# Performance work log

Measured on AMD Instinct MI355X. Metric: run time of the kernel, lower is better.

## Reference

```python
import jax, jax.numpy as jnp
import numpy as np

LAMBDA = 0.01

def setup_inputs() -> dict:
    key = jax.random.key(0)
    x = jax.random.normal(key, (32, 16384, 64), dtype=jnp.float32)
    return {"x": x}

def reference(x):
    # x: (B, N, D)
    B, N, D = x.shape
    mean = jnp.mean(x, axis=1, keepdims=True)          # (B, 1, D)
    diffs = x - mean                                    # (B, N, D)
    # Fused covariance: sum of centered outer products == GEMM, no (B,N,D,D) blowup
    cov = jnp.einsum('bnd,bne->bde', diffs, diffs) / (N - 1)  # (B, D, D)
    cov = cov + LAMBDA * jnp.eye(D, dtype=x.dtype)
    # torch.unique on the flattened symmetric matrices == globally sorted set of the
    # B * D*(D+1)/2 distinct entries (duplicates only arise from symmetry, prob-1 for
    # continuous inputs). Extract upper triangle per batch, then global sort.
    iu, ju = jnp.triu_indices(D)
    tri = cov[:, iu, ju]                                # (B, d_out)
    d_out = D * (D + 1) // 2
    return jnp.sort(tri.reshape(-1)).reshape(B, d_out)
```

## Files before the change

### kernel.cpp

```cpp
#include <hip/hip_runtime.h>
#include <stdint.h>


#define BATCHES 32
#define NSAMP   16384
#define DIM     64
#define LAMBDA  0.01f
#define NTRI    2080
#define NOUT    (BATCHES * NTRI)

#define CHUNKS_PER_BATCH 32
#define SAMP_PER_BLOCK   (NSAMP / CHUNKS_PER_BATCH)
#define SAMP_PER_WAVE    (SAMP_PER_BLOCK / 4)
#define LDS_ROW_BYTES    72
#define LDS_WAVE_BYTES   (DIM * LDS_ROW_BYTES)

typedef __attribute__((ext_vector_type(4))) float f32x4;
typedef __attribute__((ext_vector_type(8))) short s16x8;

__device__ __forceinline__ uint32_t f32_to_bf16(float f) {
    uint32_t u = __builtin_bit_cast(uint32_t, f);
    return (u + 0x7FFFu + ((u >> 16) & 1u)) >> 16;
}

__device__ __forceinline__ uint32_t sort_key(float v) {
    uint32_t u = __builtin_bit_cast(uint32_t, v);
    return u ^ (uint32_t)(((int32_t)u >> 31) | 0x80000000u);
}

__global__ __launch_bounds__(256, 4) void cov_kernel(const float* __restrict__ x,
                                                     float* __restrict__ S,
                                                     float* __restrict__ Msum) {
    __shared__ union {
        char  trans[4][LDS_WAVE_BYTES];
        float red[2][64][41];
    } lds_u;

    const int tid  = threadIdx.x;
    const int wave = tid >> 6;
    const int lane = tid & 63;
    const int b     = blockIdx.x / CHUNKS_PER_BATCH;
    const int chunk = blockIdx.x % CHUNKS_PER_BATCH;
    const int n_start = chunk * SAMP_PER_BLOCK + wave * SAMP_PER_WAVE;
    const float* xb = x + ((size_t)b * NSAMP + n_start) * DIM;

    char* lds = lds_u.trans[wave];

    const int l15  = lane & 15;
    const int quad = lane >> 4;
    char* frag_base = lds + l15 * LDS_ROW_BYTES + quad * 16;
    char* wrow = lds + lane * LDS_ROW_BYTES;

    f32x4 acc[10];
#pragma unroll
    for (int t = 0; t < 10; ++t) acc[t] = (f32x4){0.f, 0.f, 0.f, 0.f};
    float sum = 0.f;

    for (int kc = 0; kc < SAMP_PER_WAVE / 32; ++kc) {
#pragma unroll
        for (int h = 0; h < 2; ++h) {
            const float* xs = xb + (kc * 32 + h * 16) * DIM + lane;
            float v[16];
#pragma unroll
            for (int j = 0; j < 16; ++j) v[j] = xs[j * DIM];
#pragma unroll
            for (int j = 0; j < 16; ++j) sum += v[j];
            uint32_t p[8];
#pragma unroll
            for (int j = 0; j < 8; ++j)
                p[j] = f32_to_bf16(v[2 * j]) | (f32_to_bf16(v[2 * j + 1]) << 16);
#pragma unroll
            for (int j = 0; j < 4; ++j)
                *(uint2*)(wrow + h * 32 + j * 8) = make_uint2(p[2 * j], p[2 * j + 1]);
        }

        s16x8 frag[4];
#pragma unroll
        for (int t = 0; t < 4; ++t) {
            uint2 lo = *(uint2*)(frag_base + t * 16 * LDS_ROW_BYTES);
            uint2 hi = *(uint2*)(frag_base + t * 16 * LDS_ROW_BYTES + 8);
            uint4 u = make_uint4(lo.x, lo.y, hi.x, hi.y);
            frag[t] = __builtin_bit_cast(s16x8, u);
        }

        acc[0] = __builtin_amdgcn_mfma_f32_16x16x32_bf16(frag[0], frag[0], acc[0], 0, 0, 0);
        acc[1] = __builtin_amdgcn_mfma_f32_16x16x32_bf16(frag[0], frag[1], acc[1], 0, 0, 0);
        acc[2] = __builtin_amdgcn_mfma_f32_16x16x32_bf16(frag[0], frag[2], acc[2], 0, 0, 0);
        acc[3] = __builtin_amdgcn_mfma_f32_16x16x32_bf16(frag[0], frag[3], acc[3], 0, 0, 0);
        acc[4] = __builtin_amdgcn_mfma_f32_16x16x32_bf16(frag[1], frag[1], acc[4], 0, 0, 0);
        acc[5] = __builtin_amdgcn_mfma_f32_16x16x32_bf16(frag[1], frag[2], acc[5], 0, 0, 0);
        acc[6] = __builtin_amdgcn_mfma_f32_16x16x32_bf16(frag[1], frag[3], acc[6], 0, 0, 0);
        acc[7] = __builtin_amdgcn_mfma_f32_16x16x32_bf16(frag[2], frag[2], acc[7], 0, 0, 0);
        acc[8] = __builtin_amdgcn_mfma_f32_16x16x32_bf16(frag[2], frag[3], acc[8], 0, 0, 0);
        acc[9] = __builtin_amdgcn_mfma_f32_16x16x32_bf16(frag[3], frag[3], acc[9], 0, 0, 0);
    }

    __syncthreads();
    if (wave == 1 || wave == 3) {
        int slot = wave >> 1;
#pragma unroll
        for (int t = 0; t < 10; ++t)
#pragma unroll
            for (int r = 0; r < 4; ++r) lds_u.red[slot][lane][t * 4 + r] = acc[t][r];
    }
    __syncthreads();
    if (wave == 0 || wave == 2) {
        int slot = wave >> 1;
#pragma unroll
        for (int t = 0; t < 10; ++t)
#pragma unroll
            for (int r = 0; r < 4; ++r) acc[t][r] += lds_u.red[slot][lane][t * 4 + r];
    }
    __syncthreads();
    if (wave == 2) {
#pragma unroll
        for (int t = 0; t < 10; ++t)
#pragma unroll
            for (int r = 0; r < 4; ++r) lds_u.red[0][lane][t * 4 + r] = acc[t][r];
    }
    __syncthreads();

    atomicAdd(&Msum[b * DIM + lane], sum);

    if (wave == 0) {
#pragma unroll
        for (int t = 0; t < 10; ++t)
#pragma unroll
            for (int r = 0; r < 4; ++r) acc[t][r] += lds_u.red[0][lane][t * 4 + r];

        const int tmi[10] = {0, 0, 0, 0, 1, 1, 1, 2, 2, 3};
        const int tni[10] = {0, 1, 2, 3, 1, 2, 3, 2, 3, 3};
        float* Sb = S + b * DIM * DIM;
#pragma unroll
        for (int t = 0; t < 10; ++t) {
            int d0 = tmi[t] * 16 + quad * 4;
            int e  = tni[t] * 16 + l15;
#pragma unroll
            for (int r = 0; r < 4; ++r)
                atomicAdd(&Sb[(d0 + r) * DIM + e], acc[t][r]);
        }
    }
}

__global__ void finalize_kernel(const float* __restrict__ S,
                                const float* __restrict__ Msum,
                                float* __restrict__ tri,
                                uint32_t* __restrict__ hist) {
    int t = blockIdx.x * blockDim.x + threadIdx.x;
    int b = t >> 12, de = t & 4095, d = de >> 6, e = de & 63;
    if (d > e) return;
    float ssum = S[b * 4096 + d * 64 + e];
    float md = Msum[b * 64 + d], me = Msum[b * 64 + e];
    float v = (ssum - md * me * (1.0f / NSAMP)) * (1.0f / (NSAMP - 1));
    if (d == e) v += LAMBDA;
    int p = d * 64 - (d * (d + 1)) / 2 + e;
    tri[b * NTRI + p] = v;
    atomicAdd(&hist[sort_key(v) >> 16], 1u);
}

__global__ __launch_bounds__(256) void scanA_kernel(const uint32_t* __restrict__ hist,
                                                    uint32_t* __restrict__ blocksums) {
    __shared__ uint32_t s[256];
    int tid = threadIdx.x;
    s[tid] = hist[blockIdx.x * 256 + tid];
    __syncthreads();
    for (int off = 128; off > 0; off >>= 1) {
        if (tid < off) s[tid] += s[tid + off];
        __syncthreads();
    }
    if (tid == 0) blocksums[blockIdx.x] = s[0];
}

__global__ __launch_bounds__(256) void scanB_kernel(const uint32_t* __restrict__ hist,
                                                    const uint32_t* __restrict__ blocksums,
                                                    uint32_t* __restrict__ offsets,
                                                    uint2* __restrict__ wl_small,
                                                    uint2* __restrict__ wl_large,
                                                    uint32_t* __restrict__ counts) {
    __shared__ uint32_t bs[256];
    __shared__ uint32_t sc[256];
    int tid = threadIdx.x, bid = blockIdx.x;

    bs[tid] = blocksums[tid];
    __syncthreads();
    for (int off = 1; off < 256; off <<= 1) {
        uint32_t a = (tid >= off) ? bs[tid - off] : 0u;
        __syncthreads();
        bs[tid] += a;
        __syncthreads();
    }
    uint32_t base = (bid > 0) ? bs[bid - 1] : 0u;

    uint32_t v = hist[bid * 256 + tid];
    sc[tid] = v;
    __syncthreads();
    for (int off = 1; off < 256; off <<= 1) {
        uint32_t a = (tid >= off) ? sc[tid - off] : 0u;
        __syncthreads();
        sc[tid] += a;
        __syncthreads();
    }
    uint32_t excl = base + sc[tid] - v;
    offsets[bid * 256 + tid] = excl;
    if (v >= 2u) {
        if (v <= 64u) {
            uint32_t w = atomicAdd(&counts[0], 1u);
            wl_small[w] = make_uint2(excl, v);
        } else {
            uint32_t w = atomicAdd(&counts[1], 1u);
            wl_large[w] = make_uint2(excl, v);
        }
    }
}

__global__ void scatter_kernel(const float* __restrict__ tri,
                               uint32_t* __restrict__ offsets,
                               float* __restrict__ out) {
    int i = blockIdx.x * blockDim.x + threadIdx.x;
    if (i >= NOUT) return;
    float v = tri[i];
    uint32_t pos = atomicAdd(&offsets[sort_key(v) >> 16], 1u);
    out[pos] = v;
}

__global__ __launch_bounds__(256) void runsort_small_kernel(float* __restrict__ out,
                                                            const uint2* __restrict__ wl,
                                                            const uint32_t* __restrict__ counts) {
    uint32_t nw = counts[0];
    int wave = threadIdx.x >> 6, lane = threadIdx.x & 63;
    for (uint32_t r = blockIdx.x * 4 + wave; r < nw; r += gridDim.x * 4) {
        uint2 e = wl[r];
        uint32_t start = e.x, cnt = e.y;
        float v = (lane < (int)cnt) ? out[start + lane] : __builtin_inff();
#pragma unroll
        for (uint32_t k = 2; k <= 64; k <<= 1)
            for (uint32_t j = k >> 1; j > 0; j >>= 1) {
                float p = __shfl_xor(v, (int)j, 64);
                bool keepmin = (((lane & k) == 0u) == ((lane & j) == 0u));
                v = keepmin ? fminf(v, p) : fmaxf(v, p);
            }
        if (lane < (int)cnt) out[start + lane] = v;
    }
}

#define SORT_CAP 8192
__global__ __launch_bounds__(256) void runsort_large_kernel(float* __restrict__ out,
                                                            const uint2* __restrict__ wl,
                                                            const uint32_t* __restrict__ counts) {
    __shared__ float buf[SORT_CAP];
    uint32_t nw = counts[1];
    for (uint32_t w = blockIdx.x; w < nw; w += gridDim.x) {
        uint2 ent = wl[w];
        uint32_t start = ent.x, cnt = ent.y;
        if (cnt > SORT_CAP) continue;
        uint32_t m = 1;
        while (m < cnt) m <<= 1;
        for (uint32_t i = threadIdx.x; i < m; i += blockDim.x)
            buf[i] = (i < cnt) ? out[start + i] : __builtin_inff();
        __syncthreads();
        for (uint32_t k = 2; k <= m; k <<= 1) {
            for (uint32_t j = k >> 1; j > 0; j >>= 1) {
                for (uint32_t i = threadIdx.x; i < m; i += blockDim.x) {
                    uint32_t ixj = i ^ j;
                    if (ixj > i) {
                        float a = buf[i], c = buf[ixj];
                        bool up = ((i & k) == 0u);
                        if ((a > c) == up) { buf[i] = c; buf[ixj] = a; }
                    }
                }
                __syncthreads();
            }
        }
        for (uint32_t i = threadIdx.x; i < cnt; i += blockDim.x)
            out[start + i] = buf[i];
        __syncthreads();
    }
}

extern "C" void kernel_launch(void* const* d_in, const int* in_sizes, int n_in,
                              void* d_out, int out_size, void* d_ws, size_t ws_size,
                              hipStream_t stream) {
    const float* x = (const float*)d_in[0];
    float* out = (float*)d_out;
    char* ws = (char*)d_ws;

    float*    S         = (float*)(ws);
    float*    Msum      = (float*)(ws + 524288);
    uint32_t* hist      = (uint32_t*)(ws + 532480);
    uint32_t* counts    = (uint32_t*)(ws + 794624);
    uint32_t* offsets   = (uint32_t*)(ws + 794688);
    uint32_t* blocksums = (uint32_t*)(ws + 1056832);
    float*    tri       = (float*)(ws + 1057856);
    uint2*    wl_small  = (uint2*)(ws + 1324096);
    uint2*    wl_large  = (uint2*)(ws + 1590336);

    hipMemsetAsync(d_ws, 0, 794688, stream);
    cov_kernel<<<BATCHES * CHUNKS_PER_BATCH, 256, 0, stream>>>(x, S, Msum);
    finalize_kernel<<<(BATCHES * 4096) / 256, 256, 0, stream>>>(S, Msum, tri, hist);
    scanA_kernel<<<256, 256, 0, stream>>>(hist, blocksums);
    scanB_kernel<<<256, 256, 0, stream>>>(hist, blocksums, offsets, wl_small, wl_large, counts);
    scatter_kernel<<<260, 256, 0, stream>>>(tri, offsets, out);
    runsort_small_kernel<<<128, 256, 0, stream>>>(out, wl_small, counts);
    runsort_large_kernel<<<64, 256, 0, stream>>>(out, wl_large, counts);
}
```

Baseline: 366.2 us.

## Replace global atomic covariance accumulation with per-block partials and fused reduce

Each covariance block now writes its raw MFMA accumulator tile and its column sums to a private partials buffer, with no float atomics into S and Msum. A new per-batch reduce kernel sums the 32 chunk partials, applies the mean correction, scaling and lambda, and fills the triangle and histogram. This removes atomic contention, the separate finalize pass, and a larger memset. It costs an extra ~10 MB partials write and read, and the reduce runs on only 32 blocks. The old atomic path is kept as a fallback when the workspace is too small.

```diff
diff --git a/kernel.cpp b/kernel.cpp
--- a/kernel.cpp
+++ b/kernel.cpp
@@ -14,6 +14,7 @@
 #define SAMP_PER_WAVE    (SAMP_PER_BLOCK / 4)
 #define LDS_ROW_BYTES    72
 #define LDS_WAVE_BYTES   (DIM * LDS_ROW_BYTES)
+#define PARTIAL_STRIDE   2624
 
 typedef __attribute__((ext_vector_type(4))) float f32x4;
 typedef __attribute__((ext_vector_type(8))) short s16x8;
@@ -28,14 +29,20 @@
     return u ^ (uint32_t)(((int32_t)u >> 31) | 0x80000000u);
 }
 
-__global__ __launch_bounds__(256, 4) void cov_kernel(const float* __restrict__ x,
-                                                     float* __restrict__ S,
-                                                     float* __restrict__ Msum) {
-    __shared__ union {
+__constant__ const int c_tmi[10] = {0, 0, 0, 0, 1, 1, 1, 2, 2, 3};
+__constant__ const int c_tni[10] = {0, 1, 2, 3, 1, 2, 3, 2, 3, 3};
+
+struct CovLds {
+    union {
         char  trans[4][LDS_WAVE_BYTES];
         float red[2][64][41];
-    } lds_u;
-
+    } u;
+    float msum_red[4][64];
+};
+
+template <typename EpilogueFn>
+__device__ __forceinline__ void cov_body(const float* __restrict__ x, CovLds& L,
+                                         EpilogueFn epi) {
     const int tid  = threadIdx.x;
     const int wave = tid >> 6;
     const int lane = tid & 63;
@@ -44,7 +51,7 @@
     const int n_start = chunk * SAMP_PER_BLOCK + wave * SAMP_PER_WAVE;
     const float* xb = x + ((size_t)b * NSAMP + n_start) * DIM;
 
-    char* lds = lds_u.trans[wave];
+    char* lds = L.u.trans[wave];
 
     const int l15  = lane & 15;
     const int quad = lane >> 4;
@@ -95,13 +102,14 @@
         acc[9] = __builtin_amdgcn_mfma_f32_16x16x32_bf16(frag[3], frag[3], acc[9], 0, 0, 0);
     }
 
+    L.msum_red[wave][lane] = sum;
     __syncthreads();
     if (wave == 1 || wave == 3) {
         int slot = wave >> 1;
 #pragma unroll
         for (int t = 0; t < 10; ++t)
 #pragma unroll
-            for (int r = 0; r < 4; ++r) lds_u.red[slot][lane][t * 4 + r] = acc[t][r];
+            for (int r = 0; r < 4; ++r) L.u.red[slot][lane][t * 4 + r] = acc[t][r];
     }
     __syncthreads();
     if (wave == 0 || wave == 2) {
@@ -109,35 +117,90 @@
 #pragma unroll
         for (int t = 0; t < 10; ++t)
 #pragma unroll
-            for (int r = 0; r < 4; ++r) acc[t][r] += lds_u.red[slot][lane][t * 4 + r];
+            for (int r = 0; r < 4; ++r) acc[t][r] += L.u.red[slot][lane][t * 4 + r];
     }
     __syncthreads();
     if (wave == 2) {
 #pragma unroll
         for (int t = 0; t < 10; ++t)
 #pragma unroll
-            for (int r = 0; r < 4; ++r) lds_u.red[0][lane][t * 4 + r] = acc[t][r];
-    }
-    __syncthreads();
-
-    atomicAdd(&Msum[b * DIM + lane], sum);
-
+            for (int r = 0; r < 4; ++r) L.u.red[0][lane][t * 4 + r] = acc[t][r];
+    }
+    __syncthreads();
     if (wave == 0) {
 #pragma unroll
         for (int t = 0; t < 10; ++t)
 #pragma unroll
-            for (int r = 0; r < 4; ++r) acc[t][r] += lds_u.red[0][lane][t * 4 + r];
-
-        const int tmi[10] = {0, 0, 0, 0, 1, 1, 1, 2, 2, 3};
-        const int tni[10] = {0, 1, 2, 3, 1, 2, 3, 2, 3, 3};
+            for (int r = 0; r < 4; ++r) acc[t][r] += L.u.red[0][lane][t * 4 + r];
+        float msum_tot = L.msum_red[0][lane] + L.msum_red[1][lane] +
+                         L.msum_red[2][lane] + L.msum_red[3][lane];
+        epi(b, lane, quad, l15, acc, msum_tot);
+    }
+}
+
+__global__ __launch_bounds__(256, 4) void cov_kernel_p(const float* __restrict__ x,
+                                                       float* __restrict__ partials) {
+    __shared__ CovLds L;
+    float* Pb = partials + (size_t)blockIdx.x * PARTIAL_STRIDE;
+    cov_body(x, L, [&](int b, int lane, int quad, int l15, f32x4* acc, float msum) {
+#pragma unroll
+        for (int t = 0; t < 10; ++t)
+#pragma unroll
+            for (int r = 0; r < 4; ++r)
+                Pb[t * 256 + r * 64 + lane] = acc[t][r];
+        Pb[2560 + lane] = msum;
+    });
+}
+
+__global__ __launch_bounds__(256, 4) void cov_kernel_a(const float* __restrict__ x,
+                                                       float* __restrict__ S,
+                                                       float* __restrict__ Msum) {
+    __shared__ CovLds L;
+    cov_body(x, L, [&](int b, int lane, int quad, int l15, f32x4* acc, float msum) {
         float* Sb = S + b * DIM * DIM;
 #pragma unroll
         for (int t = 0; t < 10; ++t) {
-            int d0 = tmi[t] * 16 + quad * 4;
-            int e  = tni[t] * 16 + l15;
+            int d0 = c_tmi[t] * 16 + quad * 4;
+            int e  = c_tni[t] * 16 + l15;
 #pragma unroll
             for (int r = 0; r < 4; ++r)
                 atomicAdd(&Sb[(d0 + r) * DIM + e], acc[t][r]);
+        }
+        atomicAdd(&Msum[b * DIM + lane], msum);
+    });
+}
+
+__global__ __launch_bounds__(256) void reduce_kernel(const float* __restrict__ partials,
+                                                     float* __restrict__ tri,
+                                                     uint32_t* __restrict__ hist) {
+    __shared__ float msum[DIM];
+    const int b = blockIdx.x, tid = threadIdx.x;
+    const float* P0 = partials + (size_t)b * CHUNKS_PER_BATCH * PARTIAL_STRIDE;
+
+    float acc10[10];
+#pragma unroll
+    for (int k = 0; k < 10; ++k) acc10[k] = 0.f;
+    float ms = 0.f;
+    for (int c = 0; c < CHUNKS_PER_BATCH; ++c) {
+        const float* P = P0 + c * PARTIAL_STRIDE;
+#pragma unroll
+        for (int k = 0; k < 10; ++k) acc10[k] += P[tid + 256 * k];
+        if (tid < DIM) ms += P[2560 + tid];
+    }
+    if (tid < DIM) msum[tid] = ms;
+    __syncthreads();
+
+    const int r = tid >> 6, lane = tid & 63, quad = lane >> 4, l15 = lane & 15;
+#pragma unroll
+    for (int k = 0; k < 10; ++k) {
+        int row = c_tmi[k] * 16 + quad * 4 + r;
+        int col = c_tni[k] * 16 + l15;
+        if (row <= col) {
+            float v = (acc10[k] - msum[row] * msum[col] * (1.0f / NSAMP)) * (1.0f / (NSAMP - 1));
+            if (row == col) v += LAMBDA;
+            int p = row * 64 - (row * (row + 1)) / 2 + col;
+            tri[b * NTRI + p] = v;
+            atomicAdd(&hist[sort_key(v) >> 16], 1u);
         }
     }
 }
@@ -284,22 +347,44 @@
     float* out = (float*)d_out;
     char* ws = (char*)d_ws;
 
-    float*    S         = (float*)(ws);
-    float*    Msum      = (float*)(ws + 524288);
-    uint32_t* hist      = (uint32_t*)(ws + 532480);
-    uint32_t* counts    = (uint32_t*)(ws + 794624);
-    uint32_t* offsets   = (uint32_t*)(ws + 794688);
-    uint32_t* blocksums = (uint32_t*)(ws + 1056832);
-    float*    tri       = (float*)(ws + 1057856);
-    uint2*    wl_small  = (uint2*)(ws + 1324096);
-    uint2*    wl_large  = (uint2*)(ws + 1590336);
-
-    hipMemsetAsync(d_ws, 0, 794688, stream);
-    cov_kernel<<<BATCHES * CHUNKS_PER_BATCH, 256, 0, stream>>>(x, S, Msum);
-    finalize_kernel<<<(BATCHES * 4096) / 256, 256, 0, stream>>>(S, Msum, tri, hist);
-    scanA_kernel<<<256, 256, 0, stream>>>(hist, blocksums);
-    scanB_kernel<<<256, 256, 0, stream>>>(hist, blocksums, offsets, wl_small, wl_large, counts);
-    scatter_kernel<<<260, 256, 0, stream>>>(tri, offsets, out);
-    runsort_small_kernel<<<128, 256, 0, stream>>>(out, wl_small, counts);
-    runsort_large_kernel<<<64, 256, 0, stream>>>(out, wl_large, counts);
-}
+    const size_t NEED_P = 1066048 + (size_t)1024 * PARTIAL_STRIDE * 4;
+
+    if (ws_size >= NEED_P) {
+        uint32_t* hist      = (uint32_t*)(ws);
+        uint32_t* counts    = (uint32_t*)(ws + 262144);
+        uint32_t* offsets   = (uint32_t*)(ws + 262208);
+        uint32_t* blocksums = (uint32_t*)(ws + 524352);
+        float*    tri       = (float*)(ws + 525376);
+        uint2*    wl_small  = (uint2*)(ws + 791616);
+        uint2*    wl_large  = (uint2*)(ws + 1057856);
+        float*    partials  = (float*)(ws + 1066048);
+
+        hipMemsetAsync(d_ws, 0, 262208, stream);
+        cov_kernel_p<<<BATCHES * CHUNKS_PER_BATCH, 256, 0, stream>>>(x, partials);
+        reduce_kernel<<<BATCHES, 256, 0, stream>>>(partials, tri, hist);
+        scanA_kernel<<<256, 256, 0, stream>>>(hist, blocksums);
+        scanB_kernel<<<256, 256, 0, stream>>>(hist, blocksums, offsets, wl_small, wl_large, counts);
+        scatter_kernel<<<260, 256, 0, stream>>>(tri, offsets, out);
+        runsort_small_kernel<<<128, 256, 0, stream>>>(out, wl_small, counts);
+        runsort_large_kernel<<<64, 256, 0, stream>>>(out, wl_large, counts);
+    } else {
+        float*    S         = (float*)(ws);
+        float*    Msum      = (float*)(ws + 524288);
+        uint32_t* hist      = (uint32_t*)(ws + 532480);
+        uint32_t* counts    = (uint32_t*)(ws + 794624);
+        uint32_t* offsets   = (uint32_t*)(ws + 794688);
+        uint32_t* blocksums = (uint32_t*)(ws + 1056832);
+        float*    tri       = (float*)(ws + 1057856);
+        uint2*    wl_small  = (uint2*)(ws + 1324096);
+        uint2*    wl_large  = (uint2*)(ws + 1590336);
+
+        hipMemsetAsync(d_ws, 0, 794688, stream);
+        cov_kernel_a<<<BATCHES * CHUNKS_PER_BATCH, 256, 0, stream>>>(x, S, Msum);
+        finalize_kernel<<<(BATCHES * 4096) / 256, 256, 0, stream>>>(S, Msum, tri, hist);
+        scanA_kernel<<<256, 256, 0, stream>>>(hist, blocksums);
+        scanB_kernel<<<256, 256, 0, stream>>>(hist, blocksums, offsets, wl_small, wl_large, counts);
+        scatter_kernel<<<260, 256, 0, stream>>>(tri, offsets, out);
+        runsort_small_kernel<<<128, 256, 0, stream>>>(out, wl_small, counts);
+        runsort_large_kernel<<<64, 256, 0, stream>>>(out, wl_large, counts);
+    }
+}
```

New measurement: 330.8 us. 9.7% less time.
